# Kernel tuning notes

Hardware: AMD Instinct MI355X
Metric: run time of the kernel (lower is better)

The kernel has to match this reference:

```python
import jax, jax.numpy as jnp
from jax import lax
import numpy as np

EPS = 1e-5  # BatchNorm eps


def setup_inputs() -> dict:
    key = jax.random.key(0)
    ks = jax.random.split(key, 4)
    T, B, C = 256, 128, 1024
    L, H, NCLS = 6, 1024, 1000
    x = jax.random.normal(ks[0], (T, B, C), dtype=jnp.float32)
    W = jax.random.normal(ks[1], (L, C, H), dtype=jnp.float32) * (1.0 / np.sqrt(C))
    b = jnp.zeros((L, H), dtype=jnp.float32)
    gamma = jnp.ones((L, H), dtype=jnp.float32)
    beta = jnp.zeros((L, H), dtype=jnp.float32)
    u = jax.random.uniform(ks[2], (L, H), dtype=jnp.float32)  # recurrent weights in (0, U_bound~1)
    Wc = jax.random.normal(ks[3], (H, NCLS), dtype=jnp.float32) * (1.0 / np.sqrt(H))
    bc = jnp.zeros((NCLS,), dtype=jnp.float32)
    return {"x": x, "W": W, "b": b, "gamma": gamma, "beta": beta, "u": u, "Wc": Wc, "bc": bc}


def _layer(h, Wl, bl, gl, betal, ul):
    # per-timestep dense projection: [T,B,Cin] @ [Cin,H]
    z = jnp.einsum('tbi,ih->tbh', h, Wl) + bl
    # BN over (time, batch) per channel (bn_before, training-mode batch stats)
    mean = jnp.mean(z, axis=(0, 1))
    var = jnp.var(z, axis=(0, 1))
    z = (z - mean) * (gl / jnp.sqrt(var + EPS)) + betal
    # IndRNN diagonal recurrence: h_t = relu(z_t + u * h_{t-1}), h_0 = 0
    T, B, H = z.shape
    def step(hprev, zt):
        hnew = jax.nn.relu(zt + ul * hprev)
        return hnew, hnew
    _, hs = lax.scan(step, jnp.zeros((B, H), dtype=z.dtype), z)
    return hs


def reference(x, W, b, gamma, beta, u, Wc, bc):
    h = x
    for l in range(W.shape[0]):
        h = _layer(h, W[l], b[l], gamma[l], beta[l], u[l])
    # classifier on last timestep
    return h[-1] @ Wc + bc
```

## Files before the change

### kernel.cpp

```cpp
#include <hip/hip_runtime.h>
#include <hip/hip_bf16.h>

#define T_DIM 256
#define B_DIM 128
#define C_DIM 1024
#define H_DIM 1024
#define L_DIM 6
#define NC_DIM 1000
#define M_DIM (T_DIM * B_DIM)
#define BH_DIM (B_DIM * H_DIM)

typedef __attribute__((ext_vector_type(8))) short bf16x8;
typedef __attribute__((ext_vector_type(4))) float f32x4;

__device__ __forceinline__ float bf2f(unsigned short u) {
  union { unsigned int i; float f; } v; v.i = ((unsigned int)u) << 16; return v.f;
}
__device__ __forceinline__ unsigned short f2bf(float f) {
  union { float f; unsigned int i; } v; v.f = f;
  unsigned int r = v.i + 0x7fffu + ((v.i >> 16) & 1u);
  return (unsigned short)(r >> 16);
}

__device__ __forceinline__ void gload_lds16(const void* g, void* l) {
  __builtin_amdgcn_global_load_lds(
      (const __attribute__((address_space(1))) unsigned int*)g,
      (__attribute__((address_space(3))) unsigned int*)l, 16, 0, 0);
}

__global__ __launch_bounds__(256) void f32_to_bf16_kernel(
    const float* __restrict__ in, unsigned short* __restrict__ out, int n4) {
  int stride = gridDim.x * blockDim.x;
  for (int i = blockIdx.x * blockDim.x + threadIdx.x; i < n4; i += stride) {
    float4 v = ((const float4*)in)[i];
    ushort4 o;
    o.x = f2bf(v.x); o.y = f2bf(v.y); o.z = f2bf(v.z); o.w = f2bf(v.w);
    ((ushort4*)out)[i] = o;
  }
}

__global__ __launch_bounds__(256) void wtrans_kernel(
    const float* __restrict__ W, unsigned short* __restrict__ Wt) {
  __shared__ float tile[32][33];
  int l = blockIdx.z;
  const float* Wl = W + (size_t)l * C_DIM * H_DIM;
  unsigned short* Wtl = Wt + (size_t)l * C_DIM * H_DIM;
  int h0 = blockIdx.x * 32, c0 = blockIdx.y * 32;
  int tx = threadIdx.x, ty = threadIdx.y;
#pragma unroll
  for (int i = 0; i < 32; i += 8)
    tile[ty + i][tx] = Wl[(size_t)(c0 + ty + i) * H_DIM + h0 + tx];
  __syncthreads();
#pragma unroll
  for (int i = 0; i < 32; i += 8)
    Wtl[(size_t)(h0 + ty + i) * C_DIM + c0 + tx] = f2bf(tile[tx][ty + i]);
}

#define NT 32

__global__ __launch_bounds__(512, 2) void gemm_kernel(
    const unsigned short* __restrict__ A, const unsigned short* __restrict__ Bt,
    unsigned short* __restrict__ Z, float* __restrict__ psum, float* __restrict__ psqs) {
  extern __shared__ char lds[];
  int bid = blockIdx.x;
  int swz = (bid & 7) * 64 + (bid >> 3);
  int tm = swz >> 2, tn = swz & 3;
  int tid = threadIdx.x;
  int wv = tid >> 6, ln = tid & 63;
  int wm = wv >> 2, wn = wv & 3;

  const char* Asrc = (const char*)A + (size_t)tm * 256 * 2048;
  const char* Bsrc = (const char*)Bt + (size_t)tn * 256 * 2048;
  int p0 = wv * 1024 + ln * 16;
  int p1 = 8192 + wv * 1024 + ln * 16;
  int l0 = p0 ^ (((p0 >> 7) & 3) << 4);
  int l1 = p1 ^ (((p1 >> 7) & 3) << 4);
  int ro0 = (p0 >> 6) * 2048 + (l0 & 63);
  int ro1 = (p1 >> 6) * 2048 + (l1 & 63);
  int dst0 = wv * 1024;
  int dst1 = 8192 + wv * 1024;

  int laneoff = (ln & 15) * 64 + ((((ln >> 4) ^ ((ln & 15) >> 1)) & 3) << 4);

  f32x4 acc[8][4];
  f32x4 zero = {0.f, 0.f, 0.f, 0.f};
#pragma unroll
  for (int m = 0; m < 8; ++m)
#pragma unroll
    for (int n = 0; n < 4; ++n) acc[m][n] = zero;

  auto stageA = [&](int t) {
    char* ldsb = lds + ((t & 3) * 32768);
    int ko = t * 64;
    gload_lds16(Asrc + ro0 + ko, ldsb + dst0);
    gload_lds16(Asrc + ro1 + ko, ldsb + dst1);
  };
  auto stageB = [&](int t) {
    char* ldsb = lds + ((t & 3) * 32768);
    int ko = t * 64;
    gload_lds16(Bsrc + ro0 + ko, ldsb + 16384 + dst0);
    gload_lds16(Bsrc + ro1 + ko, ldsb + 16384 + dst1);
  };

  auto body = [&](int t, bool dostage) {
    const char* buf = lds + ((t & 3) * 32768);
    const char* Ab = buf + wm * 8192;
    const char* Bb = buf + 16384 + wn * 4096;
    bf16x8 bf[4], a0[4], a1[4];
#pragma unroll
    for (int n = 0; n < 4; ++n) bf[n] = *(const bf16x8*)(Bb + n * 1024 + laneoff);
#pragma unroll
    for (int m = 0; m < 4; ++m) a0[m] = *(const bf16x8*)(Ab + m * 1024 + laneoff);
    if (dostage) stageA(t + 3);
    __builtin_amdgcn_s_barrier();
    __builtin_amdgcn_s_setprio(1);
#pragma unroll
    for (int m = 0; m < 4; ++m)
#pragma unroll
      for (int n = 0; n < 4; ++n)
        acc[m][n] = __builtin_amdgcn_mfma_f32_16x16x32_bf16(a0[m], bf[n], acc[m][n], 0, 0, 0);
    __builtin_amdgcn_s_setprio(0);
    __builtin_amdgcn_s_barrier();
#pragma unroll
    for (int m = 0; m < 4; ++m) a1[m] = *(const bf16x8*)(Ab + 4096 + m * 1024 + laneoff);
    if (dostage) stageB(t + 3);
    __builtin_amdgcn_s_setprio(1);
#pragma unroll
    for (int m = 0; m < 4; ++m)
#pragma unroll
      for (int n = 0; n < 4; ++n)
        acc[m + 4][n] = __builtin_amdgcn_mfma_f32_16x16x32_bf16(a1[m], bf[n], acc[m + 4][n], 0, 0, 0);
    __builtin_amdgcn_s_setprio(0);
  };

  stageA(0); stageB(0); stageA(1); stageB(1); stageA(2); stageB(2);
  asm volatile("s_waitcnt vmcnt(8)" ::: "memory");
  __builtin_amdgcn_s_barrier();

  for (int t = 0; t < NT - 3; ++t) {
    body(t, true);
    asm volatile("s_waitcnt vmcnt(8)" ::: "memory");
    __builtin_amdgcn_s_barrier();
  }
  body(NT - 3, false);
  asm volatile("s_waitcnt vmcnt(4)" ::: "memory");
  __builtin_amdgcn_s_barrier();
  body(NT - 2, false);
  asm volatile("s_waitcnt vmcnt(0)" ::: "memory");
  __builtin_amdgcn_s_barrier();
  body(NT - 1, false);

  float s[4], q[4];
#pragma unroll
  for (int n = 0; n < 4; ++n) {
    float sv = 0.f, qv = 0.f;
#pragma unroll
    for (int m = 0; m < 8; ++m)
#pragma unroll
      for (int r = 0; r < 4; ++r) {
        float v = acc[m][n][r];
        sv += v; qv += v * v;
      }
    s[n] = sv; q[n] = qv;
  }
#pragma unroll
  for (int n = 0; n < 4; ++n) {
    s[n] += __shfl_xor(s[n], 16); s[n] += __shfl_xor(s[n], 32);
    q[n] += __shfl_xor(q[n], 16); q[n] += __shfl_xor(q[n], 32);
  }
  float* red = (float*)lds;
  if (ln < 16) {
#pragma unroll
    for (int n = 0; n < 4; ++n) {
      red[wm * 256 + wn * 64 + n * 16 + ln] = s[n];
      red[512 + wm * 256 + wn * 64 + n * 16 + ln] = q[n];
    }
  }
  __syncthreads();
  if (tid < 256) {
    psum[(size_t)tm * H_DIM + tn * 256 + tid] = red[tid] + red[256 + tid];
  } else {
    int c = tid - 256;
    psqs[(size_t)tm * H_DIM + tn * 256 + c] = red[512 + c] + red[768 + c];
  }
  int r0 = tm * 256 + wm * 128 + ((ln >> 4) << 2);
  int c0 = tn * 256 + wn * 64 + (ln & 15);
#pragma unroll
  for (int m = 0; m < 8; ++m)
#pragma unroll
    for (int n = 0; n < 4; ++n) {
      unsigned short* zp = Z + (size_t)(r0 + m * 16) * H_DIM + c0 + n * 16;
#pragma unroll
      for (int r = 0; r < 4; ++r) zp[(size_t)r * H_DIM] = f2bf(acc[m][n][r]);
    }
}

__global__ __launch_bounds__(256) void bn_finalize_kernel(
    const float* __restrict__ psum, const float* __restrict__ psqs,
    const float* __restrict__ gamma, const float* __restrict__ beta,
    float* __restrict__ ss) {
  int c = blockIdx.x * blockDim.x + threadIdx.x;
  float s = 0.f, q = 0.f;
  for (int i = 0; i < 128; ++i) {
    s += psum[(size_t)i * H_DIM + c];
    q += psqs[(size_t)i * H_DIM + c];
  }
  const float invN = 1.0f / (float)M_DIM;
  float mean = s * invN;
  float var = q * invN - mean * mean;
  float sc = gamma[c] * rsqrtf(var + 1e-5f);
  ss[c] = sc;
  ss[H_DIM + c] = beta[c] - mean * sc;
}

__global__ __launch_bounds__(256) void bn_recur_kernel(
    const unsigned short* __restrict__ Z, const float* __restrict__ ss,
    const float* __restrict__ u, unsigned short* __restrict__ Hout) {
  int i2 = blockIdx.x * 256 + threadIdx.x;
  int h0 = (i2 & (H_DIM / 2 - 1)) * 2;
  float sc0 = ss[h0], sc1 = ss[h0 + 1];
  float sh0 = ss[H_DIM + h0], sh1 = ss[H_DIM + h0 + 1];
  float u0 = u[h0], u1 = u[h0 + 1];
  float hv0 = 0.f, hv1 = 0.f;
  const size_t ST = BH_DIM / 2;
  const unsigned int* Zt = (const unsigned int*)Z + i2;
  unsigned int* Ht = (unsigned int*)Hout + i2;

  unsigned int za[32], zb[32];
#pragma unroll
  for (int j = 0; j < 32; ++j) za[j] = Zt[(size_t)j * ST];

#pragma unroll
  for (int blk = 0; blk < 4; ++blk) {
    int tA = blk * 64;
#pragma unroll
    for (int j = 0; j < 32; ++j) zb[j] = Zt[(size_t)(tA + 32 + j) * ST];
#pragma unroll
    for (int j = 0; j < 32; ++j) {
      unsigned int zz = za[j];
      float z0 = fmaf(bf2f((unsigned short)(zz & 0xffffu)), sc0, sh0);
      float z1 = fmaf(bf2f((unsigned short)(zz >> 16)), sc1, sh1);
      hv0 = fmaxf(fmaf(u0, hv0, z0), 0.f);
      hv1 = fmaxf(fmaf(u1, hv1, z1), 0.f);
      Ht[(size_t)(tA + j) * ST] = ((unsigned int)f2bf(hv1) << 16) | f2bf(hv0);
    }
    if (blk < 3) {
#pragma unroll
      for (int j = 0; j < 32; ++j) za[j] = Zt[(size_t)(tA + 64 + j) * ST];
    }
#pragma unroll
    for (int j = 0; j < 32; ++j) {
      unsigned int zz = zb[j];
      float z0 = fmaf(bf2f((unsigned short)(zz & 0xffffu)), sc0, sh0);
      float z1 = fmaf(bf2f((unsigned short)(zz >> 16)), sc1, sh1);
      hv0 = fmaxf(fmaf(u0, hv0, z0), 0.f);
      hv1 = fmaxf(fmaf(u1, hv1, z1), 0.f);
      Ht[(size_t)(tA + 32 + j) * ST] = ((unsigned int)f2bf(hv1) << 16) | f2bf(hv0);
    }
  }
}

__global__ __launch_bounds__(256) void classifier_kernel(
    const unsigned short* __restrict__ hlast, const float* __restrict__ Wc,
    const float* __restrict__ bc, float* __restrict__ out) {
  __shared__ float hs[H_DIM];
  int b = blockIdx.y;
  int n = blockIdx.x * 256 + threadIdx.x;
  for (int k = threadIdx.x; k < H_DIM; k += 256)
    hs[k] = bf2f(hlast[(size_t)b * H_DIM + k]);
  __syncthreads();
  if (n < NC_DIM) {
    float acc = bc[n];
#pragma unroll 8
    for (int k = 0; k < H_DIM; ++k)
      acc = fmaf(hs[k], Wc[(size_t)k * NC_DIM + n], acc);
    out[(size_t)b * NC_DIM + n] = acc;
  }
}

extern "C" void kernel_launch(void* const* d_in, const int* in_sizes, int n_in,
                              void* d_out, int out_size, void* d_ws, size_t ws_size,
                              hipStream_t stream) {
  const float* x     = (const float*)d_in[0];
  const float* W     = (const float*)d_in[1];
  const float* gamma = (const float*)d_in[3];
  const float* beta  = (const float*)d_in[4];
  const float* u     = (const float*)d_in[5];
  const float* Wc    = (const float*)d_in[6];
  const float* bc    = (const float*)d_in[7];
  float* out = (float*)d_out;

  const size_t CH = (size_t)C_DIM * H_DIM;
  const size_t MH = (size_t)M_DIM * H_DIM;
  char* p = (char*)d_ws;
  unsigned short* Wt = (unsigned short*)p; p += L_DIM * CH * sizeof(unsigned short);
  unsigned short* Ha = (unsigned short*)p; p += MH * sizeof(unsigned short);
  unsigned short* Hb = (unsigned short*)p; p += MH * sizeof(unsigned short);
  unsigned short* Z  = (unsigned short*)p; p += MH * sizeof(unsigned short);
  float* psum = (float*)p; p += 128 * H_DIM * sizeof(float);
  float* psqs = (float*)p; p += 128 * H_DIM * sizeof(float);
  float* ss   = (float*)p; p += 2 * H_DIM * sizeof(float);

  f32_to_bf16_kernel<<<2048, 256, 0, stream>>>(x, Ha, (int)(MH / 4));
  wtrans_kernel<<<dim3(H_DIM / 32, C_DIM / 32, L_DIM), dim3(32, 8), 0, stream>>>(W, Wt);

  unsigned short* cur = Ha;
  unsigned short* nxt = Hb;
  for (int l = 0; l < L_DIM; ++l) {
    gemm_kernel<<<(M_DIM / 256) * (H_DIM / 256), 512, 131072, stream>>>(
        cur, Wt + (size_t)l * CH, Z, psum, psqs);
    bn_finalize_kernel<<<4, 256, 0, stream>>>(psum, psqs, gamma + (size_t)l * H_DIM,
                                              beta + (size_t)l * H_DIM, ss);
    bn_recur_kernel<<<BH_DIM / 512, 256, 0, stream>>>(Z, ss, u + (size_t)l * H_DIM, nxt);
    unsigned short* tmp = cur; cur = nxt; nxt = tmp;
  }
  classifier_kernel<<<dim3(4, B_DIM), 256, 0, stream>>>(
      cur + (size_t)(T_DIM - 1) * BH_DIM, Wc, bc, out);
}
```

Before: 760.0 us.

## Switch GEMM to 32x32x16 MFMA with double-buffered fragment reads

Replaces the 16x16x32 bf16 MFMA tiling with 32x32x16 MFMA (4x2 tiles per wave), which cuts the LDS fragment reads needed per FLOP. The main loop is also rebuilt to prefetch the next K-half's fragments from LDS while MFMAs run on the current ones, with one barrier per iteration instead of three. The epilogue and BN partial-sum reductions are adapted to the 32x32 accumulator layout. The risks are higher register pressure from the extra fragment buffers and possible LDS bank conflicts under the new swizzle offsets.

```diff
diff --git a/kernel.cpp b/kernel.cpp
--- a/kernel.cpp
+++ b/kernel.cpp
@@ -11,7 +11,7 @@
 #define BH_DIM (B_DIM * H_DIM)
 
 typedef __attribute__((ext_vector_type(8))) short bf16x8;
-typedef __attribute__((ext_vector_type(4))) float f32x4;
+typedef __attribute__((ext_vector_type(16))) float f32x16;
 
 __device__ __forceinline__ float bf2f(unsigned short u) {
   union { unsigned int i; float f; } v; v.i = ((unsigned int)u) << 16; return v.f;
@@ -68,6 +68,7 @@
   int tid = threadIdx.x;
   int wv = tid >> 6, ln = tid & 63;
   int wm = wv >> 2, wn = wv & 3;
+  int lr = ln & 31;
 
   const char* Asrc = (const char*)A + (size_t)tm * 256 * 2048;
   const char* Bsrc = (const char*)Bt + (size_t)tn * 256 * 2048;
@@ -80,119 +81,107 @@
   int dst0 = wv * 1024;
   int dst1 = 8192 + wv * 1024;
 
-  int laneoff = (ln & 15) * 64 + ((((ln >> 4) ^ ((ln & 15) >> 1)) & 3) << 4);
-
-  f32x4 acc[8][4];
-  f32x4 zero = {0.f, 0.f, 0.f, 0.f};
-#pragma unroll
-  for (int m = 0; m < 8; ++m)
-#pragma unroll
-    for (int n = 0; n < 4; ++n) acc[m][n] = zero;
+  int swzk = (lr >> 1) & 3;
+  int loff0 = lr * 64 + ((((ln >> 5)) ^ swzk) << 4);
+  int loff1 = lr * 64 + ((((ln >> 5) + 2) ^ swzk) << 4);
+
+  f32x16 acc[4][2];
+#pragma unroll
+  for (int m = 0; m < 4; ++m)
+#pragma unroll
+    for (int n = 0; n < 2; ++n)
+#pragma unroll
+      for (int r = 0; r < 16; ++r) acc[m][n][r] = 0.f;
 
   auto stageA = [&](int t) {
-    char* ldsb = lds + ((t & 3) * 32768);
-    int ko = t * 64;
-    gload_lds16(Asrc + ro0 + ko, ldsb + dst0);
-    gload_lds16(Asrc + ro1 + ko, ldsb + dst1);
+    char* b = lds + ((t & 3) * 32768); int ko = t * 64;
+    gload_lds16(Asrc + ro0 + ko, b + dst0);
+    gload_lds16(Asrc + ro1 + ko, b + dst1);
   };
   auto stageB = [&](int t) {
-    char* ldsb = lds + ((t & 3) * 32768);
-    int ko = t * 64;
-    gload_lds16(Bsrc + ro0 + ko, ldsb + 16384 + dst0);
-    gload_lds16(Bsrc + ro1 + ko, ldsb + 16384 + dst1);
+    char* b = lds + ((t & 3) * 32768); int ko = t * 64;
+    gload_lds16(Bsrc + ro0 + ko, b + 16384 + dst0);
+    gload_lds16(Bsrc + ro1 + ko, b + 16384 + dst1);
   };
 
-  auto body = [&](int t, bool dostage) {
+  bf16x8 a0[4], b0[2], a1[4], b1[2];
+  auto readf = [&](int t, int loff, bf16x8* a, bf16x8* b) {
     const char* buf = lds + ((t & 3) * 32768);
     const char* Ab = buf + wm * 8192;
     const char* Bb = buf + 16384 + wn * 4096;
-    bf16x8 bf[4], a0[4], a1[4];
-#pragma unroll
-    for (int n = 0; n < 4; ++n) bf[n] = *(const bf16x8*)(Bb + n * 1024 + laneoff);
-#pragma unroll
-    for (int m = 0; m < 4; ++m) a0[m] = *(const bf16x8*)(Ab + m * 1024 + laneoff);
-    if (dostage) stageA(t + 3);
-    __builtin_amdgcn_s_barrier();
+#pragma unroll
+    for (int m = 0; m < 4; ++m) a[m] = *(const bf16x8*)(Ab + m * 2048 + loff);
+#pragma unroll
+    for (int n = 0; n < 2; ++n) b[n] = *(const bf16x8*)(Bb + n * 2048 + loff);
+  };
+  auto domfma = [&](bf16x8* a, bf16x8* b) {
     __builtin_amdgcn_s_setprio(1);
 #pragma unroll
     for (int m = 0; m < 4; ++m)
 #pragma unroll
-      for (int n = 0; n < 4; ++n)
-        acc[m][n] = __builtin_amdgcn_mfma_f32_16x16x32_bf16(a0[m], bf[n], acc[m][n], 0, 0, 0);
-    __builtin_amdgcn_s_setprio(0);
-    __builtin_amdgcn_s_barrier();
-#pragma unroll
-    for (int m = 0; m < 4; ++m) a1[m] = *(const bf16x8*)(Ab + 4096 + m * 1024 + laneoff);
-    if (dostage) stageB(t + 3);
-    __builtin_amdgcn_s_setprio(1);
-#pragma unroll
-    for (int m = 0; m < 4; ++m)
-#pragma unroll
-      for (int n = 0; n < 4; ++n)
-        acc[m + 4][n] = __builtin_amdgcn_mfma_f32_16x16x32_bf16(a1[m], bf[n], acc[m + 4][n], 0, 0, 0);
+      for (int n = 0; n < 2; ++n)
+        acc[m][n] = __builtin_amdgcn_mfma_f32_32x32x16_bf16(a[m], b[n], acc[m][n], 0, 0, 0);
     __builtin_amdgcn_s_setprio(0);
   };
 
   stageA(0); stageB(0); stageA(1); stageB(1); stageA(2); stageB(2);
-  asm volatile("s_waitcnt vmcnt(8)" ::: "memory");
-  __builtin_amdgcn_s_barrier();
-
-  for (int t = 0; t < NT - 3; ++t) {
-    body(t, true);
-    asm volatile("s_waitcnt vmcnt(8)" ::: "memory");
-    __builtin_amdgcn_s_barrier();
-  }
-  body(NT - 3, false);
   asm volatile("s_waitcnt vmcnt(4)" ::: "memory");
   __builtin_amdgcn_s_barrier();
-  body(NT - 2, false);
-  asm volatile("s_waitcnt vmcnt(0)" ::: "memory");
-  __builtin_amdgcn_s_barrier();
-  body(NT - 1, false);
-
-  float s[4], q[4];
-#pragma unroll
-  for (int n = 0; n < 4; ++n) {
+  readf(0, loff0, a0, b0);
+
+  for (int t = 0; t < NT; ++t) {
+    if (t <= NT - 4) stageA(t + 3);
+    readf(t, loff1, a1, b1);
+    domfma(a0, b0);
+    if (t <= NT - 4) stageB(t + 3);
+    if (t < NT - 1) readf(t + 1, loff0, a0, b0);
+    domfma(a1, b1);
+    if (t < NT - 1) {
+      if (t <= NT - 4) { asm volatile("s_waitcnt vmcnt(4)" ::: "memory"); }
+      else             { asm volatile("s_waitcnt vmcnt(0)" ::: "memory"); }
+      __builtin_amdgcn_s_barrier();
+    }
+  }
+
+  float s[2], q[2];
+#pragma unroll
+  for (int n = 0; n < 2; ++n) {
     float sv = 0.f, qv = 0.f;
 #pragma unroll
-    for (int m = 0; m < 8; ++m)
-#pragma unroll
-      for (int r = 0; r < 4; ++r) {
-        float v = acc[m][n][r];
-        sv += v; qv += v * v;
-      }
+    for (int m = 0; m < 4; ++m)
+#pragma unroll
+      for (int r = 0; r < 16; ++r) { float v = acc[m][n][r]; sv += v; qv += v * v; }
     s[n] = sv; q[n] = qv;
   }
 #pragma unroll
-  for (int n = 0; n < 4; ++n) {
-    s[n] += __shfl_xor(s[n], 16); s[n] += __shfl_xor(s[n], 32);
-    q[n] += __shfl_xor(q[n], 16); q[n] += __shfl_xor(q[n], 32);
-  }
+  for (int n = 0; n < 2; ++n) { s[n] += __shfl_xor(s[n], 32); q[n] += __shfl_xor(q[n], 32); }
   float* red = (float*)lds;
-  if (ln < 16) {
-#pragma unroll
-    for (int n = 0; n < 4; ++n) {
-      red[wm * 256 + wn * 64 + n * 16 + ln] = s[n];
-      red[512 + wm * 256 + wn * 64 + n * 16 + ln] = q[n];
+  if (ln < 32) {
+#pragma unroll
+    for (int n = 0; n < 2; ++n) {
+      red[wm * 256 + wn * 64 + n * 32 + lr] = s[n];
+      red[512 + wm * 256 + wn * 64 + n * 32 + lr] = q[n];
     }
   }
   __syncthreads();
   if (tid < 256) {
     psum[(size_t)tm * H_DIM + tn * 256 + tid] = red[tid] + red[256 + tid];
-  } else {
+  } else if (tid < 512) {
     int c = tid - 256;
     psqs[(size_t)tm * H_DIM + tn * 256 + c] = red[512 + c] + red[768 + c];
   }
-  int r0 = tm * 256 + wm * 128 + ((ln >> 4) << 2);
-  int c0 = tn * 256 + wn * 64 + (ln & 15);
-#pragma unroll
-  for (int m = 0; m < 8; ++m)
-#pragma unroll
-    for (int n = 0; n < 4; ++n) {
-      unsigned short* zp = Z + (size_t)(r0 + m * 16) * H_DIM + c0 + n * 16;
-#pragma unroll
-      for (int r = 0; r < 4; ++r) zp[(size_t)r * H_DIM] = f2bf(acc[m][n][r]);
-    }
+  int colb = tn * 256 + wn * 64 + lr;
+  int rowb = tm * 256 + wm * 128 + ((ln >> 5) << 2);
+#pragma unroll
+  for (int m = 0; m < 4; ++m)
+#pragma unroll
+    for (int n = 0; n < 2; ++n)
+#pragma unroll
+      for (int g = 0; g < 4; ++g) {
+        unsigned short* zp = Z + (size_t)(rowb + m * 32 + 8 * g) * H_DIM + colb + n * 32;
+#pragma unroll
+        for (int r = 0; r < 4; ++r) zp[(size_t)r * H_DIM] = f2bf(acc[m][n][4 * g + r]);
+      }
 }
 
 __global__ __launch_bounds__(256) void bn_finalize_kernel(
```

After: 772.7 us. No clear change (+1.7%).

## Restructure GEMM main loop to double-buffered 128-wide K tiles with finer staging

Applied to the files above, without the earlier changes.

The GEMM main loop now uses two 64KB LDS buffers, each holding a 128-wide K slab split into four 16KB regions (A and B for two k-halves), in place of a four-deep ring of 64-wide K tiles. Each iteration interleaves four staged global-to-LDS loads with four MFMA quarter-blocks, and adds explicit barriers, lgkmcnt waits and sched_barriers. The aim is to cut per-iteration barrier and loop overhead and to overlap loads with MFMA work more finely. The cost is a shallower prefetch distance (one tile ahead instead of three), more barriers per iteration, and a different LDS swizzle mapping that has to match the fragment reads.

```diff
diff --git a/kernel.cpp b/kernel.cpp
--- a/kernel.cpp
+++ b/kernel.cpp
@@ -56,7 +56,7 @@
     Wtl[(size_t)(h0 + ty + i) * C_DIM + c0 + tx] = f2bf(tile[tx][ty + i]);
 }
 
-#define NT 32
+#define NT 16
 
 __global__ __launch_bounds__(512, 2) void gemm_kernel(
     const unsigned short* __restrict__ A, const unsigned short* __restrict__ Bt,
@@ -69,18 +69,27 @@
   int wv = tid >> 6, ln = tid & 63;
   int wm = wv >> 2, wn = wv & 3;
 
-  const char* Asrc = (const char*)A + (size_t)tm * 256 * 2048;
-  const char* Bsrc = (const char*)Bt + (size_t)tn * 256 * 2048;
-  int p0 = wv * 1024 + ln * 16;
-  int p1 = 8192 + wv * 1024 + ln * 16;
-  int l0 = p0 ^ (((p0 >> 7) & 3) << 4);
-  int l1 = p1 ^ (((p1 >> 7) & 3) << 4);
-  int ro0 = (p0 >> 6) * 2048 + (l0 & 63);
-  int ro1 = (p1 >> 6) * 2048 + (l1 & 63);
-  int dst0 = wv * 1024;
-  int dst1 = 8192 + wv * 1024;
-
-  int laneoff = (ln & 15) * 64 + ((((ln >> 4) ^ ((ln & 15) >> 1)) & 3) << 4);
+  const char* Apanel = (const char*)A + (size_t)tm * 256 * 2048;
+  const char* Bpanel = (const char*)Bt + (size_t)tn * 256 * 2048;
+
+  int srow0 = wv * 16 + (ln >> 2);
+  int skey = (ln >> 3) & 3;
+  int sclog = (ln & 3) ^ skey;
+  size_t soff0 = (size_t)srow0 * 2048 + sclog * 16;
+  size_t soff1 = (size_t)(128 + srow0) * 2048 + sclog * 16;
+  int sdst = wv * 1024;
+
+  auto stage = [&](int t, int region) {
+    char* base = lds + ((t & 1) * 65536) + region * 16384;
+    const char* src = (region < 2) ? Apanel : Bpanel;
+    int kb = t * 128 + (region & 1) * 64;
+    gload_lds16(src + soff0 + kb, base + sdst);
+    gload_lds16(src + soff1 + kb, base + 8192 + sdst);
+  };
+
+  int frow = ln & 15;
+  int fchunk = ((ln >> 4) ^ (frow >> 1)) & 3;
+  int floff = frow * 64 + (fchunk << 4);
 
   f32x4 acc[8][4];
   f32x4 zero = {0.f, 0.f, 0.f, 0.f};
@@ -89,66 +98,65 @@
 #pragma unroll
     for (int n = 0; n < 4; ++n) acc[m][n] = zero;
 
-  auto stageA = [&](int t) {
-    char* ldsb = lds + ((t & 3) * 32768);
-    int ko = t * 64;
-    gload_lds16(Asrc + ro0 + ko, ldsb + dst0);
-    gload_lds16(Asrc + ro1 + ko, ldsb + dst1);
+  bf16x8 bfr[4], af[4];
+  auto readB = [&](int t, int kk) {
+    const char* Bb = lds + ((t & 1) * 65536) + 32768 + kk * 16384 + wn * 4096;
+#pragma unroll
+    for (int n = 0; n < 4; ++n) bfr[n] = *(const bf16x8*)(Bb + n * 1024 + floff);
   };
-  auto stageB = [&](int t) {
-    char* ldsb = lds + ((t & 3) * 32768);
-    int ko = t * 64;
-    gload_lds16(Bsrc + ro0 + ko, ldsb + 16384 + dst0);
-    gload_lds16(Bsrc + ro1 + ko, ldsb + 16384 + dst1);
+  auto readA = [&](int t, int kk, int mq) {
+    const char* Ab = lds + ((t & 1) * 65536) + kk * 16384 + wm * 8192 + mq * 4096;
+#pragma unroll
+    for (int i = 0; i < 4; ++i) af[i] = *(const bf16x8*)(Ab + i * 1024 + floff);
   };
-
-  auto body = [&](int t, bool dostage) {
-    const char* buf = lds + ((t & 3) * 32768);
-    const char* Ab = buf + wm * 8192;
-    const char* Bb = buf + 16384 + wn * 4096;
-    bf16x8 bf[4], a0[4], a1[4];
-#pragma unroll
-    for (int n = 0; n < 4; ++n) bf[n] = *(const bf16x8*)(Bb + n * 1024 + laneoff);
-#pragma unroll
-    for (int m = 0; m < 4; ++m) a0[m] = *(const bf16x8*)(Ab + m * 1024 + laneoff);
-    if (dostage) stageA(t + 3);
-    __builtin_amdgcn_s_barrier();
+  auto mfma16 = [&](int mq) {
     __builtin_amdgcn_s_setprio(1);
 #pragma unroll
-    for (int m = 0; m < 4; ++m)
+    for (int i = 0; i < 4; ++i)
 #pragma unroll
       for (int n = 0; n < 4; ++n)
-        acc[m][n] = __builtin_amdgcn_mfma_f32_16x16x32_bf16(a0[m], bf[n], acc[m][n], 0, 0, 0);
-    __builtin_amdgcn_s_setprio(0);
-    __builtin_amdgcn_s_barrier();
-#pragma unroll
-    for (int m = 0; m < 4; ++m) a1[m] = *(const bf16x8*)(Ab + 4096 + m * 1024 + laneoff);
-    if (dostage) stageB(t + 3);
-    __builtin_amdgcn_s_setprio(1);
-#pragma unroll
-    for (int m = 0; m < 4; ++m)
-#pragma unroll
-      for (int n = 0; n < 4; ++n)
-        acc[m + 4][n] = __builtin_amdgcn_mfma_f32_16x16x32_bf16(a1[m], bf[n], acc[m + 4][n], 0, 0, 0);
+        acc[mq * 4 + i][n] =
+            __builtin_amdgcn_mfma_f32_16x16x32_bf16(af[i], bfr[n], acc[mq * 4 + i][n], 0, 0, 0);
     __builtin_amdgcn_s_setprio(0);
   };
 
-  stageA(0); stageB(0); stageA(1); stageB(1); stageA(2); stageB(2);
-  asm volatile("s_waitcnt vmcnt(8)" ::: "memory");
-  __builtin_amdgcn_s_barrier();
-
-  for (int t = 0; t < NT - 3; ++t) {
-    body(t, true);
-    asm volatile("s_waitcnt vmcnt(8)" ::: "memory");
-    __builtin_amdgcn_s_barrier();
-  }
-  body(NT - 3, false);
+  stage(0, 2); stage(0, 0); stage(0, 3); stage(0, 1);
   asm volatile("s_waitcnt vmcnt(4)" ::: "memory");
   __builtin_amdgcn_s_barrier();
-  body(NT - 2, false);
-  asm volatile("s_waitcnt vmcnt(0)" ::: "memory");
-  __builtin_amdgcn_s_barrier();
-  body(NT - 1, false);
+
+  for (int t = 0; t < NT; ++t) {
+    bool st = (t + 1 < NT);
+    readB(t, 0); readA(t, 0, 0);
+    if (st) stage(t + 1, 2);
+    __builtin_amdgcn_s_barrier();
+    asm volatile("s_waitcnt lgkmcnt(0)" ::: "memory");
+    __builtin_amdgcn_sched_barrier(0);
+    mfma16(0);
+    __builtin_amdgcn_s_barrier();
+    readA(t, 0, 1);
+    if (st) stage(t + 1, 0);
+    __builtin_amdgcn_s_barrier();
+    asm volatile("s_waitcnt lgkmcnt(0)" ::: "memory");
+    __builtin_amdgcn_sched_barrier(0);
+    mfma16(1);
+    asm volatile("s_waitcnt vmcnt(4)" ::: "memory");
+    __builtin_amdgcn_s_barrier();
+    readB(t, 1); readA(t, 1, 0);
+    if (st) stage(t + 1, 3);
+    __builtin_amdgcn_s_barrier();
+    asm volatile("s_waitcnt lgkmcnt(0)" ::: "memory");
+    __builtin_amdgcn_sched_barrier(0);
+    mfma16(0);
+    __builtin_amdgcn_s_barrier();
+    readA(t, 1, 1);
+    if (st) stage(t + 1, 1);
+    __builtin_amdgcn_s_barrier();
+    asm volatile("s_waitcnt lgkmcnt(0)" ::: "memory");
+    __builtin_amdgcn_sched_barrier(0);
+    mfma16(1);
+    asm volatile("s_waitcnt vmcnt(4)" ::: "memory");
+    __builtin_amdgcn_s_barrier();
+  }
 
   float s[4], q[4];
 #pragma unroll
```

New measurement: 761.5 us. About the same (+0.2%).
